# Performance work log

Hardware: AMD Instinct MI355X
Metric: run time of the kernel (lower is better)

## Reference

```python
import jax, jax.numpy as jnp
import numpy as np

NC, K, SD = 8, 1024, 64
L = NC * SD
B = 8192
TAU = 0.07
COMMIT_W = 1.0
CONTRAST_W = 1.0
EPS = 1e-12


def setup_inputs() -> dict:
    key = jax.random.key(0)
    kz, ke = jax.random.split(key)
    z = jax.random.normal(kz, (B, L), dtype=jnp.float32)
    embeddings = jax.random.normal(ke, (NC, K, SD), dtype=jnp.float32)
    return {"z": z, "embeddings": embeddings}


def reference(z, embeddings):
    sg = jax.lax.stop_gradient
    Bn, Ln = z.shape
    nc, k, sd = embeddings.shape
    zr = z.reshape(Bn, nc, sd)  # (B, nc, sd)

    # squared distances via ||z||^2 - 2 z.e + ||e||^2 -> (B, nc, K), avoids (B,nc,K,sd)
    z2 = jnp.sum(zr * zr, axis=-1)[:, :, None]
    e2 = jnp.sum(embeddings * embeddings, axis=-1)[None, :, :]
    cross = jnp.einsum('bnd,nkd->bnk', zr, embeddings)
    dists = z2 - 2.0 * cross + e2
    indices = jnp.argmin(dists, axis=-1)  # (B, nc)

    # codebook gather
    quant_splits = embeddings[jnp.arange(nc)[None, :], indices]  # (B, nc, sd)
    quant_z = quant_splits.reshape(Bn, Ln)

    commit_loss = jnp.mean((sg(quant_z) - z) ** 2)
    embed_loss = jnp.mean((quant_z - sg(z)) ** 2)
    total_commit = commit_loss + embed_loss

    quant_z_st = z + sg(quant_z - z)

    z_norm = z / jnp.maximum(jnp.linalg.norm(z, axis=-1, keepdims=True), EPS)
    q_det = sg(quant_z)
    q_norm = q_det / jnp.maximum(jnp.linalg.norm(q_det, axis=-1, keepdims=True), EPS)
    logits = jnp.matmul(q_norm, z_norm.T) / TAU  # (B, B)
    # cross-entropy with labels = arange(B)
    contrastive = jnp.mean(jax.nn.logsumexp(logits, axis=1) - jnp.diagonal(logits))

    return (quant_z_st, COMMIT_W * total_commit, CONTRAST_W * contrastive, indices)
```

## Files before the change

### kernel.cpp

```cpp
#include <hip/hip_runtime.h>
#include <cstdint>
#include <cstddef>

#define NCB   8
#define KC    1024
#define SDIM  64
#define LDIM  512
#define BATCH 8192
#define INV_TAU (1.0f/0.07f)
#define K2E  20.60992915555662f
#define DBIAS 256.0f

typedef __bf16 bf16_t;
typedef bf16_t bf16x8 __attribute__((ext_vector_type(8)));
typedef float  floatx4 __attribute__((ext_vector_type(4)));
typedef int    intx8  __attribute__((ext_vector_type(8)));
typedef unsigned int u32;

__device__ __forceinline__ unsigned short f2bf(float f) {
    union { float f; unsigned int u; } c; c.f = f;
    unsigned int u = c.u;
    u += 0x7fffu + ((u >> 16) & 1u);
    return (unsigned short)(u >> 16);
}
__device__ __forceinline__ float bf2f(unsigned short h) {
    union { unsigned int u; float f; } c; c.u = ((unsigned int)h) << 16;
    return c.f;
}
__device__ __forceinline__ float exp2_fast(float x) {
    float r; asm("v_exp_f32 %0, %1" : "=v"(r) : "v"(x)); return r;
}
__device__ __forceinline__ void gll16(const void* g, void* l) {
    __builtin_amdgcn_global_load_lds(
        (const __attribute__((address_space(1))) u32*)g,
        (__attribute__((address_space(3))) u32*)l,
        16, 0, 0);
}

__global__ __launch_bounds__(256) void
k_pre(const float* __restrict__ emb, float* __restrict__ e2,
      unsigned short* __restrict__ eh, unsigned short* __restrict__ el,
      float* __restrict__ accs) {
    int gid = blockIdx.x * 256 + threadIdx.x;
    int row = gid >> 3, g = gid & 7;
    const float4* e4 = (const float4*)(emb + (size_t)row*SDIM + g*8);
    float4 a = e4[0], b = e4[1];
    union { ushort4 u4[2]; uint4 v; } H, L;
    H.u4[0].x=f2bf(a.x); L.u4[0].x=f2bf(a.x-bf2f(H.u4[0].x));
    H.u4[0].y=f2bf(a.y); L.u4[0].y=f2bf(a.y-bf2f(H.u4[0].y));
    H.u4[0].z=f2bf(a.z); L.u4[0].z=f2bf(a.z-bf2f(H.u4[0].z));
    H.u4[0].w=f2bf(a.w); L.u4[0].w=f2bf(a.w-bf2f(H.u4[0].w));
    H.u4[1].x=f2bf(b.x); L.u4[1].x=f2bf(b.x-bf2f(H.u4[1].x));
    H.u4[1].y=f2bf(b.y); L.u4[1].y=f2bf(b.y-bf2f(H.u4[1].y));
    H.u4[1].z=f2bf(b.z); L.u4[1].z=f2bf(b.z-bf2f(H.u4[1].z));
    H.u4[1].w=f2bf(b.w); L.u4[1].w=f2bf(b.w-bf2f(H.u4[1].w));
    *(uint4*)(eh + (size_t)row*SDIM + g*8) = H.v;
    *(uint4*)(el + (size_t)row*SDIM + g*8) = L.v;
    float s = a.x*a.x + a.y*a.y + a.z*a.z + a.w*a.w
            + b.x*b.x + b.y*b.y + b.z*b.z + b.w*b.w;
    s += __shfl_xor(s, 1); s += __shfl_xor(s, 2); s += __shfl_xor(s, 4);
    if (g == 0) e2[row] = s;
    if (gid == 0){ accs[0]=0.f; accs[1]=0.f; accs[2]=0.f; }
}

__device__ __forceinline__ double dist64d(const float* __restrict__ e,
                                          const float* __restrict__ zg) {
    double se=0.0, sz=0.0;
#pragma unroll 8
    for (int i=0;i<64;i++){ double ev=(double)e[i];
        se = fma(ev,ev,se); sz = fma(ev,(double)zg[i],sz); }
    return se - 2.0*sz;
}

__global__ __launch_bounds__(256,2) void
k_argmin(const unsigned short* __restrict__ eh, const unsigned short* __restrict__ el,
         const float* __restrict__ e2, const float* __restrict__ z,
         const float* __restrict__ emb, float* __restrict__ out_q,
         float* __restrict__ out_idx, float* __restrict__ accs) {
    __shared__ __align__(16) unsigned short Ah[128*64], Al[128*64];
    __shared__ __align__(16) unsigned short Bh[2][64*64], Bl[2][64*64];
    __shared__ float e2s[2][64];
    __shared__ unsigned int mK[2][128][2];

    const int tid = threadIdx.x;
    const int n   = blockIdx.x & 7;
    const int i0  = (((blockIdx.x >> 3) << 3) + blockIdx.y) * 128;
    const int wid = tid >> 6, lane = tid & 63;
    const int wm = wid & 1, wn = wid >> 1;
    const int c  = lane & 15, qq = lane >> 4;

#pragma unroll
    for (int s=0;s<8;s++){
        int seg = tid + s*256;
        int r = seg >> 4, sg = seg & 15;
        float4 v = *(const float4*)(z + (size_t)(i0+r)*LDIM + n*SDIM + sg*4);
        ushort4 h, l;
        h.x=f2bf(v.x); l.x=f2bf(v.x-bf2f(h.x));
        h.y=f2bf(v.y); l.y=f2bf(v.y-bf2f(h.y));
        h.z=f2bf(v.z); l.z=f2bf(v.z-bf2f(h.z));
        h.w=f2bf(v.w); l.w=f2bf(v.w-bf2f(h.w));
        int off = r*64 + ((sg*4) ^ ((r&7)<<3));
        *(ushort4*)(&Ah[off]) = h;
        *(ushort4*)(&Al[off]) = l;
    }

    const unsigned char* ehb = (const unsigned char*)(eh + (size_t)n*KC*SDIM);
    const unsigned char* elb = (const unsigned char*)(el + (size_t)n*KC*SDIM);
    const float* e2n = e2 + n*KC;

    const int brow = lane >> 3;
    const int bchk = ((lane & 7)*16) ^ (brow << 4);

    auto stageB = [&](int buf, int j0){
#pragma unroll
        for (int s=0;s<2;s++){
            int r0 = wid*16 + s*8;
            size_t go = (size_t)(j0 + r0 + brow)*128 + bchk;
            gll16(ehb + go, &Bh[buf][r0*64]);
            gll16(elb + go, &Bl[buf][r0*64]);
        }
    };

    if (tid < 64) e2s[0][tid] = e2n[tid] + DBIAS;
    stageB(0, 0);

    unsigned int k1[16], k2[16];
#pragma unroll
    for (int j=0;j<16;j++){ k1[j]=0xFFFFFFFFu; k2[j]=0xFFFFFFFFu; }

    __syncthreads();

    for (int jt=0; jt<16; jt++){
        const int cur = jt & 1, nxt = cur ^ 1;
        const int j0 = jt*64;
        float e2r = 0.f;
        if (jt < 15){
            stageB(nxt, j0 + 64);
            if (tid < 64) e2r = e2n[j0 + 64 + tid];
        }

        floatx4 acc[4][2];
#pragma unroll
        for (int mt=0;mt<4;mt++){
            acc[mt][0]=(floatx4){0.f,0.f,0.f,0.f};
            acc[mt][1]=(floatx4){0.f,0.f,0.f,0.f};
        }

#pragma unroll
        for (int t=0;t<2;t++){
            const int axo = (t*32 + qq*8) ^ ((c&7)<<3);
            bf16x8 ah[4], alo[4], bh[2], bl[2];
#pragma unroll
            for (int mt=0;mt<4;mt++){
                int ro = (wm*64 + mt*16 + c)*64 + axo;
                ah[mt]  = *(const bf16x8*)(&Ah[ro]);
                alo[mt] = *(const bf16x8*)(&Al[ro]);
            }
#pragma unroll
            for (int nt=0;nt<2;nt++){
                int ro = (wn*32 + nt*16 + c)*64 + axo;
                bh[nt] = *(const bf16x8*)(&Bh[cur][ro]);
                bl[nt] = *(const bf16x8*)(&Bl[cur][ro]);
            }
#pragma unroll
            for (int mt=0;mt<4;mt++)
#pragma unroll
                for (int nt=0;nt<2;nt++){
                    acc[mt][nt] = __builtin_amdgcn_mfma_f32_16x16x32_bf16(ah[mt],  bh[nt], acc[mt][nt], 0,0,0);
                    acc[mt][nt] = __builtin_amdgcn_mfma_f32_16x16x32_bf16(ah[mt],  bl[nt], acc[mt][nt], 0,0,0);
                    acc[mt][nt] = __builtin_amdgcn_mfma_f32_16x16x32_bf16(alo[mt], bh[nt], acc[mt][nt], 0,0,0);
                }
        }

#pragma unroll
        for (int nt=0;nt<2;nt++){
            const int colb = wn*32 + nt*16 + c;
            float e2v = e2s[cur][colb];
            unsigned int kidx = (unsigned int)(j0 + colb);
#pragma unroll
            for (int mt=0;mt<4;mt++)
#pragma unroll
                for (int reg=0;reg<4;reg++){
                    float d = fmaf(-2.0f, acc[mt][nt][reg], e2v);
                    unsigned int key = (__float_as_uint(d) & 0xFFFFFC00u) | kidx;
                    int s = mt*4+reg;
                    unsigned int o1 = k1[s], o2 = k2[s];
                    unsigned int nk2;
                    asm("v_med3_u32 %0, %1, %2, %3" : "=v"(nk2) : "v"(o1), "v"(o2), "v"(key));
                    k2[s] = nk2;
                    k1[s] = min(o1, key);
                }
        }

        if (jt < 15 && tid < 64) e2s[nxt][tid] = e2r + DBIAS;
        __syncthreads();
    }

#pragma unroll
    for (int off=1; off<16; off<<=1){
#pragma unroll
        for (int s=0;s<16;s++){
            unsigned int o1 = __shfl_xor(k1[s], off);
            unsigned int o2 = __shfl_xor(k2[s], off);
            unsigned int n1 = min(k1[s], o1);
            k2[s] = min( max(k1[s], o1), min(k2[s], o2) );
            k1[s] = n1;
        }
    }
    if (c == 0){
#pragma unroll
        for (int s=0;s<16;s++){
            int row = wm*64 + (s>>2)*16 + qq*4 + (s&3);
            mK[wn][row][0] = k1[s]; mK[wn][row][1] = k2[s];
        }
    }
    __syncthreads();

    if (tid < 128){
        int b = i0 + tid;
        unsigned int a1 = mK[0][tid][0], a2 = mK[0][tid][1];
        unsigned int c1 = mK[1][tid][0], c2 = mK[1][tid][1];
        unsigned int f1 = min(a1, c1);
        unsigned int f2 = min( max(a1, c1), min(a2, c2) );
        int ii1 = (int)(f1 & 0x3FFu);
        int ii2 = (int)(f2 & 0x3FFu);
        float d1q = __uint_as_float(f1 & 0xFFFFFC00u);
        float d2q = __uint_as_float(f2 & 0xFFFFFC00u);

        const float* eb = emb + (size_t)n*KC*SDIM;
        const float* zg = z + (size_t)b*LDIM + n*SDIM;
        if (d2q - d1q < 0.08f) {
            double d1 = dist64d(eb + (size_t)ii1*SDIM, zg);
            double d2 = dist64d(eb + (size_t)ii2*SDIM, zg);
            if (d2 < d1 || (d2 == d1 && ii2 < ii1)) ii1 = ii2;
        }

        const float4* q4 = (const float4*)(eb + (size_t)ii1*SDIM);
        const float4* z4 = (const float4*)zg;
        float4* oq = (float4*)(out_q + (size_t)b*LDIM + n*SDIM);
        float cs = 0.f;
#pragma unroll
        for (int i=0;i<16;i++){
            float4 v = q4[i]; float4 zv = z4[i];
            oq[i] = v;
            float d0=v.x-zv.x, d1=v.y-zv.y, d2=v.z-zv.z, d3=v.w-zv.w;
            cs += d0*d0 + d1*d1 + d2*d2 + d3*d3;
        }
        out_idx[b*NCB + n] = (float)ii1;

        for (int off=32; off; off>>=1) cs += __shfl_down(cs, off);
        if ((tid & 63)==0) atomicAdd(&accs[0], cs);
    }
}

__global__ __launch_bounds__(256) void
k_norm(const float* __restrict__ z, const float* __restrict__ q,
       unsigned char* __restrict__ zn8, unsigned char* __restrict__ qn8,
       float* __restrict__ diag) {
    const int wid = threadIdx.x >> 6, lane = threadIdx.x & 63;
    const int b = blockIdx.x*4 + wid;
    const size_t base = (size_t)b*LDIM;
    const float4* z4 = (const float4*)(z + base + lane*8);
    const float4* q4 = (const float4*)(q + base + lane*8);
    float4 za = z4[0], zb = z4[1];
    float4 qa = q4[0], qb = q4[1];
    float sz = za.x*za.x + za.y*za.y + za.z*za.z + za.w*za.w
             + zb.x*zb.x + zb.y*zb.y + zb.z*zb.z + zb.w*zb.w;
    float sq = qa.x*qa.x + qa.y*qa.y + qa.z*qa.z + qa.w*qa.w
             + qb.x*qb.x + qb.y*qb.y + qb.z*qb.z + qb.w*qb.w;
    float sqz= qa.x*za.x + qa.y*za.y + qa.z*za.z + qa.w*za.w
             + qb.x*zb.x + qb.y*zb.y + qb.z*zb.z + qb.w*zb.w;
#pragma unroll
    for (int off=1; off<64; off<<=1){
        sz  += __shfl_xor(sz,  off);
        sq  += __shfl_xor(sq,  off);
        sqz += __shfl_xor(sqz, off);
    }
    float inz = 1.0f/fmaxf(sqrtf(sz), 1e-12f);
    float inq = 1.0f/fmaxf(sqrtf(sq), 1e-12f);
    if (lane == 0) diag[b] = sqz*inz*inq*INV_TAU;

    int z0 = __builtin_amdgcn_cvt_pk_fp8_f32(za.x*inz, za.y*inz, 0, false);
    z0     = __builtin_amdgcn_cvt_pk_fp8_f32(za.z*inz, za.w*inz, z0, true);
    int z1 = __builtin_amdgcn_cvt_pk_fp8_f32(zb.x*inz, zb.y*inz, 0, false);
    z1     = __builtin_amdgcn_cvt_pk_fp8_f32(zb.z*inz, zb.w*inz, z1, true);
    int q0 = __builtin_amdgcn_cvt_pk_fp8_f32(qa.x*inq, qa.y*inq, 0, false);
    q0     = __builtin_amdgcn_cvt_pk_fp8_f32(qa.z*inq, qa.w*inq, q0, true);
    int q1 = __builtin_amdgcn_cvt_pk_fp8_f32(qb.x*inq, qb.y*inq, 0, false);
    q1     = __builtin_amdgcn_cvt_pk_fp8_f32(qb.z*inq, qb.w*inq, q1, true);
    uint2 uz; uz.x = (unsigned)z0; uz.y = (unsigned)z1;
    uint2 uq; uq.x = (unsigned)q0; uq.y = (unsigned)q1;
    *(uint2*)(zn8 + base + lane*8) = uz;
    *(uint2*)(qn8 + base + lane*8) = uq;
}

__global__ __launch_bounds__(256,4) void
k_logits(const unsigned char* __restrict__ qn8, const unsigned char* __restrict__ zn8,
         float* __restrict__ Spart) {
    __shared__ __align__(16) unsigned char Bs[2][32*512];
    const int tid  = threadIdx.x;
    const int chnk = (blockIdx.x & 7) + ((blockIdx.y & 1) << 3);
    const int i0   = (((blockIdx.x >> 3) << 3) + (blockIdx.y >> 1)) * 128;
    const int wid  = tid >> 6, lane = tid & 63;
    const int wm = wid;
    const int c  = lane & 15, qq = lane >> 4;

    const int brow  = lane >> 5;
    const int bchk0 = (lane & 31) * 16;

    auto stageB = [&](int buf, int j0){
#pragma unroll
        for (int s=0;s<4;s++){
            int r0  = wid*8 + s*2;
            int row = r0 + brow;
            gll16(zn8 + (size_t)(j0+row)*LDIM + (bchk0 ^ ((row&7)<<4)),
                  &Bs[buf][r0*512]);
        }
    };

    stageB(0, chnk*512);

    intx8 af[2][4];
#pragma unroll
    for (int mt=0;mt<2;mt++){
        const unsigned char* ap = qn8 + (size_t)(i0 + wm*32 + mt*16 + c)*LDIM + qq*32;
#pragma unroll
        for (int kc=0;kc<4;kc++){
            union { intx8 v; uint4 h[2]; } u;
            u.h[0] = *(const uint4*)(ap + kc*128);
            u.h[1] = *(const uint4*)(ap + kc*128 + 16);
            af[mt][kc] = u.v;
        }
    }
#pragma unroll
    for (int mt=0;mt<2;mt++)
#pragma unroll
        for (int kc=0;kc<4;kc++)
            asm volatile("" : "+v"(af[mt][kc]));

    float S[8];
#pragma unroll
    for (int i=0;i<8;i++) S[i] = 0.f;

    __syncthreads();

    for (int jt=0;jt<16;jt++){
        const int cur = jt & 1;
        const int j0 = chnk*512 + jt*32;
        if (jt < 15) stageB(cur^1, j0 + 32);

        floatx4 acc[2][2];
#pragma unroll
        for (int mt=0;mt<2;mt++){
            acc[mt][0]=(floatx4){0.f,0.f,0.f,0.f};
            acc[mt][1]=(floatx4){0.f,0.f,0.f,0.f};
        }

#pragma unroll
        for (int kc=0;kc<4;kc++)
#pragma unroll
            for (int nt=0;nt<2;nt++){
                const int rb = nt*16 + c;
                const unsigned char* p = &Bs[cur][rb*512];
                const int o = kc*128 + qq*32;
                const int x = (rb&7)<<4;
                union { intx8 v; uint4 h[2]; } u;
                u.h[0] = *(const uint4*)(p + (o ^ x));
                u.h[1] = *(const uint4*)(p + ((o + 16) ^ x));
                intx8 bfr = u.v;
#pragma unroll
                for (int mt=0;mt<2;mt++)
                    acc[mt][nt] = __builtin_amdgcn_mfma_scale_f32_16x16x128_f8f6f4(
                        af[mt][kc], bfr, acc[mt][nt],
                        0, 0,
                        0, 127,
                        0, 127);
            }

#pragma unroll
        for (int mt=0;mt<2;mt++)
#pragma unroll
            for (int reg=0;reg<4;reg++){
                float e0 = exp2_fast(fmaf(acc[mt][0][reg], K2E, -K2E));
                float e1 = exp2_fast(fmaf(acc[mt][1][reg], K2E, -K2E));
                S[mt*4+reg] += e0 + e1;
            }
        __syncthreads();
    }

#pragma unroll
    for (int off=1; off<16; off<<=1)
#pragma unroll
        for (int s=0;s<8;s++) S[s] += __shfl_xor(S[s], off);

    if (c == 0){
        const int p = chnk;
#pragma unroll
        for (int mt=0;mt<2;mt++)
#pragma unroll
            for (int reg=0;reg<4;reg++){
                int row = i0 + wm*32 + mt*16 + qq*4 + reg;
                Spart[p*BATCH + row] = S[mt*4+reg];
            }
    }
}

__global__ __launch_bounds__(256) void
k_finalize(const float* __restrict__ Spart, const float* __restrict__ diag,
           float* __restrict__ accs, float* __restrict__ out_s) {
    int r = blockIdx.x*256 + threadIdx.x;
    float Ssum = 0.f;
#pragma unroll
    for (int p=0;p<16;p++) Ssum += Spart[p*BATCH + r];
    float val = INV_TAU + logf(Ssum) - diag[r];
    for (int off=32; off; off>>=1) val += __shfl_down(val, off);
    if ((threadIdx.x & 63)==0) atomicAdd(&accs[1], val);
    __syncthreads();
    if (threadIdx.x == 0){
        __threadfence();
        unsigned int old = __float_as_uint(atomicAdd(&accs[2], 1.0f));
        if (old == __float_as_uint(31.0f)) {
            __threadfence();
            float a0 = atomicAdd(&accs[0], 0.0f);
            float a1 = atomicAdd(&accs[1], 0.0f);
            out_s[0] = 2.0f*a0 / (float)((size_t)BATCH*LDIM);
            out_s[1] = a1 / (float)BATCH;
        }
    }
}

extern "C" void kernel_launch(void* const* d_in, const int* in_sizes, int n_in,
                              void* d_out, int out_size, void* d_ws, size_t ws_size,
                              hipStream_t stream) {
    const float* z   = (const float*)d_in[0];
    const float* emb = (const float*)d_in[1];
    float* out = (float*)d_out;
    float* out_q       = out;
    float* out_scalars = out + 4194304;
    float* out_idx     = out + 4194306;

    float* wsf   = (float*)d_ws;
    float* e2    = wsf;
    float* accs  = wsf + 8192;
    float* diag  = wsf + 8704;
    float* Spart = wsf + 16896;
    unsigned char* qn8 = (unsigned char*)(Spart + 32*BATCH);
    unsigned char* zn8 = qn8 + (size_t)BATCH*LDIM;
    unsigned short* eh = (unsigned short*)(zn8 + (size_t)BATCH*LDIM);
    unsigned short* el = eh + (size_t)NCB*KC*SDIM;

    k_pre    <<<256,         256, 0, stream>>>(emb, e2, eh, el, accs);
    k_argmin <<<dim3(64,8),  256, 0, stream>>>(eh, el, e2, z, emb,
                                               out_q, out_idx, accs);
    k_norm   <<<2048,        256, 0, stream>>>(z, out_q, zn8, qn8, diag);
    k_logits <<<dim3(64,16), 256, 0, stream>>>(qn8, zn8, Spart);
    k_finalize<<<32,         256, 0, stream>>>(Spart, diag, accs, out_scalars);
}
```

Before: 158.8 us.

## Enlarge argmin tile to 256 rows with triple-buffered codebook staging

The argmin kernel now uses 512-thread blocks covering 256 batch rows instead of 128, halving the grid. Codebook tiles move from double to triple buffering, with loads issued two tiles ahead and an explicit vmcnt wait plus raw barrier replacing __syncthreads. All 1024 e2 values are preloaded into shared memory once instead of per tile. The aim is more reuse of each staged codebook tile and more latency hiding, at the cost of larger shared memory, one block per CU, and fewer blocks in flight.

```diff
diff --git a/kernel.cpp b/kernel.cpp
--- a/kernel.cpp
+++ b/kernel.cpp
@@ -72,26 +72,43 @@
     return se - 2.0*sz;
 }
 
-__global__ __launch_bounds__(256,2) void
+__global__ __launch_bounds__(512,1) void
 k_argmin(const unsigned short* __restrict__ eh, const unsigned short* __restrict__ el,
          const float* __restrict__ e2, const float* __restrict__ z,
          const float* __restrict__ emb, float* __restrict__ out_q,
          float* __restrict__ out_idx, float* __restrict__ accs) {
-    __shared__ __align__(16) unsigned short Ah[128*64], Al[128*64];
-    __shared__ __align__(16) unsigned short Bh[2][64*64], Bl[2][64*64];
-    __shared__ float e2s[2][64];
-    __shared__ unsigned int mK[2][128][2];
+    __shared__ __align__(16) unsigned short Ah[256*64], Al[256*64];
+    __shared__ __align__(16) unsigned short Bh[3][64*64], Bl[3][64*64];
+    __shared__ float e2s[1024];
+    __shared__ unsigned int mK[2][256][2];
 
     const int tid = threadIdx.x;
     const int n   = blockIdx.x & 7;
-    const int i0  = (((blockIdx.x >> 3) << 3) + blockIdx.y) * 128;
+    const int i0  = ((blockIdx.x >> 3) | (blockIdx.y << 2)) * 256;
     const int wid = tid >> 6, lane = tid & 63;
-    const int wm = wid & 1, wn = wid >> 1;
+    const int wm = wid & 3, wn = wid >> 2;
     const int c  = lane & 15, qq = lane >> 4;
 
+    const unsigned char* ehb = (const unsigned char*)(eh + (size_t)n*KC*SDIM);
+    const unsigned char* elb = (const unsigned char*)(el + (size_t)n*KC*SDIM);
+    const float* e2n = e2 + n*KC;
+
+    const int brow = lane >> 3;
+    const int bchk = ((lane & 7)*16) ^ (brow << 4);
+
+    auto stageB = [&](int buf, int j0){
+        int r0 = wid*8;
+        size_t go = (size_t)(j0 + r0 + brow)*128 + bchk;
+        gll16(ehb + go, &Bh[buf][r0*64]);
+        gll16(elb + go, &Bl[buf][r0*64]);
+    };
+
+    stageB(0, 0);
+    stageB(1, 64);
+
 #pragma unroll
     for (int s=0;s<8;s++){
-        int seg = tid + s*256;
+        int seg = tid + s*512;
         int r = seg >> 4, sg = seg & 15;
         float4 v = *(const float4*)(z + (size_t)(i0+r)*LDIM + n*SDIM + sg*4);
         ushort4 h, l;
@@ -103,26 +120,8 @@
         *(ushort4*)(&Ah[off]) = h;
         *(ushort4*)(&Al[off]) = l;
     }
-
-    const unsigned char* ehb = (const unsigned char*)(eh + (size_t)n*KC*SDIM);
-    const unsigned char* elb = (const unsigned char*)(el + (size_t)n*KC*SDIM);
-    const float* e2n = e2 + n*KC;
-
-    const int brow = lane >> 3;
-    const int bchk = ((lane & 7)*16) ^ (brow << 4);
-
-    auto stageB = [&](int buf, int j0){
-#pragma unroll
-        for (int s=0;s<2;s++){
-            int r0 = wid*16 + s*8;
-            size_t go = (size_t)(j0 + r0 + brow)*128 + bchk;
-            gll16(ehb + go, &Bh[buf][r0*64]);
-            gll16(elb + go, &Bl[buf][r0*64]);
-        }
-    };
-
-    if (tid < 64) e2s[0][tid] = e2n[tid] + DBIAS;
-    stageB(0, 0);
+    e2s[tid]       = e2n[tid]       + DBIAS;
+    e2s[tid + 512] = e2n[tid + 512] + DBIAS;
 
     unsigned int k1[16], k2[16];
 #pragma unroll
@@ -131,13 +130,9 @@
     __syncthreads();
 
     for (int jt=0; jt<16; jt++){
-        const int cur = jt & 1, nxt = cur ^ 1;
+        const int cur = jt % 3;
         const int j0 = jt*64;
-        float e2r = 0.f;
-        if (jt < 15){
-            stageB(nxt, j0 + 64);
-            if (tid < 64) e2r = e2n[j0 + 64 + tid];
-        }
+        if (jt < 14) stageB((jt+2)%3, j0 + 128);
 
         floatx4 acc[4][2];
 #pragma unroll
@@ -175,7 +170,7 @@
 #pragma unroll
         for (int nt=0;nt<2;nt++){
             const int colb = wn*32 + nt*16 + c;
-            float e2v = e2s[cur][colb];
+            float e2v = e2s[j0 + colb];
             unsigned int kidx = (unsigned int)(j0 + colb);
 #pragma unroll
             for (int mt=0;mt<4;mt++)
@@ -192,8 +187,11 @@
                 }
         }
 
-        if (jt < 15 && tid < 64) e2s[nxt][tid] = e2r + DBIAS;
-        __syncthreads();
+        if (jt < 14) { asm volatile("s_waitcnt vmcnt(2)" ::: "memory"); }
+        else         { asm volatile("s_waitcnt vmcnt(0)" ::: "memory"); }
+        __builtin_amdgcn_sched_barrier(0);
+        __builtin_amdgcn_s_barrier();
+        __builtin_amdgcn_sched_barrier(0);
     }
 
 #pragma unroll
@@ -216,7 +214,7 @@
     }
     __syncthreads();
 
-    if (tid < 128){
+    if (tid < 256){
         int b = i0 + tid;
         unsigned int a1 = mK[0][tid][0], a2 = mK[0][tid][1];
         unsigned int c1 = mK[1][tid][0], c2 = mK[1][tid][1];
@@ -450,7 +448,7 @@
     unsigned short* el = eh + (size_t)NCB*KC*SDIM;
 
     k_pre    <<<256,         256, 0, stream>>>(emb, e2, eh, el, accs);
-    k_argmin <<<dim3(64,8),  256, 0, stream>>>(eh, el, e2, z, emb,
+    k_argmin <<<dim3(32,8),  512, 0, stream>>>(eh, el, e2, z, emb,
                                                out_q, out_idx, accs);
     k_norm   <<<2048,        256, 0, stream>>>(z, out_q, zn8, qn8, diag);
     k_logits <<<dim3(64,16), 256, 0, stream>>>(qn8, zn8, Spart);
```

Result: slower. 167.2 us (+5.3%).

## Split codebook across waves in argmin, load B fragments directly to registers

Applied to the files above, without the earlier changes.

The argmin kernel now uses 64-row z tiles per block, with each of the four waves scanning a disjoint 256-entry slice of the codebook. Codebook hi/lo fragments are loaded straight from global memory into double-buffered registers, replacing the LDS staging and the per-tile block barriers. Per-wave top-2 results are merged across four waves at the end, and the grid doubles to keep the same coverage. This removes the synchronisation and LDS traffic but adds register pressure and redundant global/L2 reads of the codebook per block.

```diff
diff --git a/kernel.cpp b/kernel.cpp
--- a/kernel.cpp
+++ b/kernel.cpp
@@ -77,20 +77,18 @@
          const float* __restrict__ e2, const float* __restrict__ z,
          const float* __restrict__ emb, float* __restrict__ out_q,
          float* __restrict__ out_idx, float* __restrict__ accs) {
-    __shared__ __align__(16) unsigned short Ah[128*64], Al[128*64];
-    __shared__ __align__(16) unsigned short Bh[2][64*64], Bl[2][64*64];
-    __shared__ float e2s[2][64];
-    __shared__ unsigned int mK[2][128][2];
+    __shared__ __align__(16) unsigned short Ah[64*64], Al[64*64];
+    __shared__ float e2s[1024];
+    __shared__ unsigned int mK[4][64][2];
 
     const int tid = threadIdx.x;
     const int n   = blockIdx.x & 7;
-    const int i0  = (((blockIdx.x >> 3) << 3) + blockIdx.y) * 128;
+    const int i0  = ((blockIdx.x >> 3) | (blockIdx.y << 4)) * 64;
     const int wid = tid >> 6, lane = tid & 63;
-    const int wm = wid & 1, wn = wid >> 1;
     const int c  = lane & 15, qq = lane >> 4;
 
 #pragma unroll
-    for (int s=0;s<8;s++){
+    for (int s=0;s<4;s++){
         int seg = tid + s*256;
         int r = seg >> 4, sg = seg & 15;
         float4 v = *(const float4*)(z + (size_t)(i0+r)*LDIM + n*SDIM + sg*4);
@@ -104,39 +102,50 @@
         *(ushort4*)(&Al[off]) = l;
     }
 
-    const unsigned char* ehb = (const unsigned char*)(eh + (size_t)n*KC*SDIM);
-    const unsigned char* elb = (const unsigned char*)(el + (size_t)n*KC*SDIM);
+    const unsigned short* ehn = eh + (size_t)n*KC*SDIM;
+    const unsigned short* eln = el + (size_t)n*KC*SDIM;
     const float* e2n = e2 + n*KC;
 
-    const int brow = lane >> 3;
-    const int bchk = ((lane & 7)*16) ^ (brow << 4);
-
-    auto stageB = [&](int buf, int j0){
-#pragma unroll
-        for (int s=0;s<2;s++){
-            int r0 = wid*16 + s*8;
-            size_t go = (size_t)(j0 + r0 + brow)*128 + bchk;
-            gll16(ehb + go, &Bh[buf][r0*64]);
-            gll16(elb + go, &Bl[buf][r0*64]);
-        }
-    };
-
-    if (tid < 64) e2s[0][tid] = e2n[tid] + DBIAS;
-    stageB(0, 0);
+#pragma unroll
+    for (int s=0;s<4;s++){
+        int idx = tid + s*256;
+        e2s[idx] = e2n[idx] + DBIAS;
+    }
 
     unsigned int k1[16], k2[16];
 #pragma unroll
     for (int j=0;j<16;j++){ k1[j]=0xFFFFFFFFu; k2[j]=0xFFFFFFFFu; }
 
+    const int jb = wid * 256;
+
+    bf16x8 bhb[2][2][2], blb[2][2][2];
+#pragma unroll
+    for (int nt=0;nt<2;nt++){
+        const size_t rb = (size_t)(jb + nt*16 + c) * SDIM;
+#pragma unroll
+        for (int t=0;t<2;t++){
+            bhb[0][nt][t] = *(const bf16x8*)(ehn + rb + t*32 + qq*8);
+            blb[0][nt][t] = *(const bf16x8*)(eln + rb + t*32 + qq*8);
+        }
+    }
+
     __syncthreads();
 
-    for (int jt=0; jt<16; jt++){
+#pragma unroll
+    for (int jt=0; jt<8; jt++){
         const int cur = jt & 1, nxt = cur ^ 1;
-        const int j0 = jt*64;
-        float e2r = 0.f;
-        if (jt < 15){
-            stageB(nxt, j0 + 64);
-            if (tid < 64) e2r = e2n[j0 + 64 + tid];
+        const int j0 = jb + jt*32;
+
+        if (jt < 7){
+#pragma unroll
+            for (int nt=0;nt<2;nt++){
+                const size_t rb = (size_t)(j0 + 32 + nt*16 + c) * SDIM;
+#pragma unroll
+                for (int t=0;t<2;t++){
+                    bhb[nxt][nt][t] = *(const bf16x8*)(ehn + rb + t*32 + qq*8);
+                    blb[nxt][nt][t] = *(const bf16x8*)(eln + rb + t*32 + qq*8);
+                }
+            }
         }
 
         floatx4 acc[4][2];
@@ -149,34 +158,28 @@
 #pragma unroll
         for (int t=0;t<2;t++){
             const int axo = (t*32 + qq*8) ^ ((c&7)<<3);
-            bf16x8 ah[4], alo[4], bh[2], bl[2];
+            bf16x8 ah[4], alo[4];
 #pragma unroll
             for (int mt=0;mt<4;mt++){
-                int ro = (wm*64 + mt*16 + c)*64 + axo;
+                int ro = (mt*16 + c)*64 + axo;
                 ah[mt]  = *(const bf16x8*)(&Ah[ro]);
                 alo[mt] = *(const bf16x8*)(&Al[ro]);
             }
 #pragma unroll
-            for (int nt=0;nt<2;nt++){
-                int ro = (wn*32 + nt*16 + c)*64 + axo;
-                bh[nt] = *(const bf16x8*)(&Bh[cur][ro]);
-                bl[nt] = *(const bf16x8*)(&Bl[cur][ro]);
-            }
-#pragma unroll
             for (int mt=0;mt<4;mt++)
 #pragma unroll
                 for (int nt=0;nt<2;nt++){
-                    acc[mt][nt] = __builtin_amdgcn_mfma_f32_16x16x32_bf16(ah[mt],  bh[nt], acc[mt][nt], 0,0,0);
-                    acc[mt][nt] = __builtin_amdgcn_mfma_f32_16x16x32_bf16(ah[mt],  bl[nt], acc[mt][nt], 0,0,0);
-                    acc[mt][nt] = __builtin_amdgcn_mfma_f32_16x16x32_bf16(alo[mt], bh[nt], acc[mt][nt], 0,0,0);
+                    acc[mt][nt] = __builtin_amdgcn_mfma_f32_16x16x32_bf16(ah[mt],  bhb[cur][nt][t], acc[mt][nt], 0,0,0);
+                    acc[mt][nt] = __builtin_amdgcn_mfma_f32_16x16x32_bf16(ah[mt],  blb[cur][nt][t], acc[mt][nt], 0,0,0);
+                    acc[mt][nt] = __builtin_amdgcn_mfma_f32_16x16x32_bf16(alo[mt], bhb[cur][nt][t], acc[mt][nt], 0,0,0);
                 }
         }
 
 #pragma unroll
         for (int nt=0;nt<2;nt++){
-            const int colb = wn*32 + nt*16 + c;
-            float e2v = e2s[cur][colb];
-            unsigned int kidx = (unsigned int)(j0 + colb);
+            const int colb = j0 + nt*16 + c;
+            float e2v = e2s[colb];
+            unsigned int kidx = (unsigned int)colb;
 #pragma unroll
             for (int mt=0;mt<4;mt++)
 #pragma unroll
@@ -191,9 +194,6 @@
                     k1[s] = min(o1, key);
                 }
         }
-
-        if (jt < 15 && tid < 64) e2s[nxt][tid] = e2r + DBIAS;
-        __syncthreads();
     }
 
 #pragma unroll
@@ -210,18 +210,22 @@
     if (c == 0){
 #pragma unroll
         for (int s=0;s<16;s++){
-            int row = wm*64 + (s>>2)*16 + qq*4 + (s&3);
-            mK[wn][row][0] = k1[s]; mK[wn][row][1] = k2[s];
+            int row = (s>>2)*16 + qq*4 + (s&3);
+            mK[wid][row][0] = k1[s]; mK[wid][row][1] = k2[s];
         }
     }
     __syncthreads();
 
-    if (tid < 128){
+    if (tid < 64){
         int b = i0 + tid;
-        unsigned int a1 = mK[0][tid][0], a2 = mK[0][tid][1];
-        unsigned int c1 = mK[1][tid][0], c2 = mK[1][tid][1];
-        unsigned int f1 = min(a1, c1);
-        unsigned int f2 = min( max(a1, c1), min(a2, c2) );
+        unsigned int f1 = mK[0][tid][0], f2 = mK[0][tid][1];
+#pragma unroll
+        for (int w=1; w<4; w++){
+            unsigned int b1 = mK[w][tid][0], b2 = mK[w][tid][1];
+            unsigned int n1 = min(f1, b1);
+            f2 = min( max(f1, b1), min(f2, b2) );
+            f1 = n1;
+        }
         int ii1 = (int)(f1 & 0x3FFu);
         int ii2 = (int)(f2 & 0x3FFu);
         float d1q = __uint_as_float(f1 & 0xFFFFFC00u);
@@ -249,7 +253,7 @@
         out_idx[b*NCB + n] = (float)ii1;
 
         for (int off=32; off; off>>=1) cs += __shfl_down(cs, off);
-        if ((tid & 63)==0) atomicAdd(&accs[0], cs);
+        if (tid == 0) atomicAdd(&accs[0], cs);
     }
 }
 
@@ -450,7 +454,7 @@
     unsigned short* el = eh + (size_t)NCB*KC*SDIM;
 
     k_pre    <<<256,         256, 0, stream>>>(emb, e2, eh, el, accs);
-    k_argmin <<<dim3(64,8),  256, 0, stream>>>(eh, el, e2, z, emb,
+    k_argmin <<<dim3(128,8), 256, 0, stream>>>(eh, el, e2, z, emb,
                                                out_q, out_idx, accs);
     k_norm   <<<2048,        256, 0, stream>>>(z, out_q, zn8, qn8, diag);
     k_logits <<<dim3(64,16), 256, 0, stream>>>(qn8, zn8, Spart);
```

Result: no change. 161.9 us (+1.9%).
